# Performance work log

Hardware: AMD Instinct MI355X
Metric: run time of the kernel (lower is better)

## Reference

```python
import jax, jax.numpy as jnp
import numpy as np

B, N, E = 8, 4096, 1024
H = 16
D = E // H
NMAX = 4096
N_FFT = NMAX // 2 + 1  # 2049
HIDDEN = max(32, D)    # 64
LN_EPS = 1e-5


def setup_inputs() -> dict:
    key = jax.random.key(0)
    ks = jax.random.split(key, 8)
    s = 0.02
    return {
        "x": jax.random.normal(ks[0], (B, N, E), jnp.float32),
        "positions": jnp.arange(N, dtype=jnp.int64),
        "Wq": jax.random.normal(ks[1], (E, E), jnp.float32) * s,
        "Wv": jax.random.normal(ks[2], (E, E), jnp.float32) * s,
        "Wo": jax.random.normal(ks[3], (E, E), jnp.float32) * s,
        "ln_g": jnp.ones((D,), jnp.float32),
        "ln_b": jnp.zeros((D,), jnp.float32),
        "w1": jax.random.normal(ks[4], (HIDDEN, D), jnp.float32) * s,
        "b1": jnp.zeros((HIDDEN,), jnp.float32),
        "w2": jax.random.normal(ks[5], (2 * N_FFT, HIDDEN), jnp.float32) * s,
        "b2": jnp.zeros((2 * N_FFT,), jnp.float32),
    }


def _build_gate(bar_q, ln_g, ln_b, w1, b1, w2, b2):
    # bar_q: (B,H,D) -> complex gate (B,H,n_fft)
    mu = bar_q.mean(-1, keepdims=True)
    var = ((bar_q - mu) ** 2).mean(-1, keepdims=True)  # biased var (torch LayerNorm)
    h = (bar_q - mu) * jax.lax.rsqrt(var + LN_EPS) * ln_g + ln_b
    h = jax.nn.silu(h @ w1.T + b1)                      # (B,H,HIDDEN)
    g = (h @ w2.T + b2).reshape(bar_q.shape[0], H, N_FFT, 2)
    return jax.lax.complex(g[..., 0], g[..., 1])        # (B,H,n_fft)


def reference(x, positions, Wq, Wv, Wo, ln_g, ln_b, w1, b1, w2, b2):
    b, n, e = x.shape
    q = (x @ Wq.T).reshape(b, n, H, D).transpose(0, 2, 1, 3)  # (B,H,N,D)
    v = (x @ Wv.T).reshape(b, n, H, D).transpose(0, 2, 1, 3)  # (B,H,N,D)
    v_fft = jnp.fft.rfft(v, axis=2)                            # (B,H,n_fft,D) complex
    bar_q = q.mean(axis=2)                                     # (B,H,D)
    gate = _build_gate(bar_q, ln_g, ln_b, w1, b1, w2, b2)      # (B,H,n_fft)
    spec = v_fft * gate[..., None]
    seq_full = jnp.fft.irfft(spec, n=NMAX, axis=2)             # (B,H,Nmax,D)
    v_sel = jnp.take(seq_full, positions, axis=2)              # (B,H,N,D)
    v_out = v_sel.transpose(0, 2, 1, 3).reshape(b, n, e)
    return v_out @ Wo.T
```

## Files before the change

kernel.cpp:

```cpp
#include <hip/hip_runtime.h>
#include <cstdint>

#define B_   8
#define N_   4096
#define E_   1024
#define H_   16
#define NFFT 2049

typedef unsigned short u16;
typedef unsigned int   u32;
typedef __attribute__((ext_vector_type(4))) float f32x4;
typedef __attribute__((ext_vector_type(8))) short short8;

__device__ __forceinline__ u16 f2bf(float f) {
    u32 u = __builtin_bit_cast(u32, f);
    u += 0x7fffu + ((u >> 16) & 1u);
    return (u16)(u >> 16);
}
__device__ __forceinline__ float bf2f(u16 h) {
    u32 u = ((u32)h) << 16;
    return __builtin_bit_cast(float, u);
}

__global__ __launch_bounds__(256)
void conv_x_kernel(const float* __restrict__ x, u16* __restrict__ xbf,
                   float* __restrict__ xbar)
{
    const int b  = blockIdx.y;
    const int n0 = blockIdx.x * 64;
    const int t  = threadIdx.x;
    const float4* src = (const float4*)(x + ((size_t)(b * N_ + n0)) * E_) + t;
    u16* dst = xbf + ((size_t)(b * N_ + n0)) * E_ + t * 4;
    float4 s = make_float4(0.f, 0.f, 0.f, 0.f);
    for (int r = 0; r < 64; r++) {
        float4 v = src[r * 256];
        s.x += v.x; s.y += v.y; s.z += v.z; s.w += v.w;
        *(ushort4*)(dst + (size_t)r * E_) =
            make_ushort4(f2bf(v.x), f2bf(v.y), f2bf(v.z), f2bf(v.w));
    }
    float* xb = xbar + b * E_ + t * 4;
    atomicAdd(xb + 0, s.x); atomicAdd(xb + 1, s.y);
    atomicAdd(xb + 2, s.z); atomicAdd(xb + 3, s.w);
}

__global__ __launch_bounds__(256)
void convw_kernel(const float* __restrict__ w, u16* __restrict__ wbf, int n4)
{
    int i = blockIdx.x * 256 + threadIdx.x;
    if (i >= n4) return;
    float4 v = ((const float4*)w)[i];
    *(ushort4*)(wbf + (size_t)i * 4) =
        make_ushort4(f2bf(v.x), f2bf(v.y), f2bf(v.z), f2bf(v.w));
}

__global__ __launch_bounds__(256)
void gate_kernel(const float* __restrict__ xbar, const float* __restrict__ Wq,
                 const float* __restrict__ ln_g, const float* __restrict__ ln_b,
                 const float* __restrict__ w1,   const float* __restrict__ b1,
                 const float* __restrict__ w2,   const float* __restrict__ b2,
                 float* __restrict__ gate)
{
    const int bh = blockIdx.x;
    const int b = bh >> 4, h = bh & 15;
    const int t = threadIdx.x;
    __shared__ float s_x[1024];
    __shared__ float s_bq[64], s_ln[64], s_h1[64];

    for (int q = 0; q < 4; q++)
        s_x[(q << 8) + t] = xbar[b * 1024 + (q << 8) + t] * (1.0f / 4096.0f);
    __syncthreads();

    {
        const int d = t >> 2, part = t & 3;
        const float* wrow = Wq + (size_t)(h * 64 + d) * 1024 + part * 256;
        const float* xr = s_x + part * 256;
        float sum = 0.f;
        #pragma unroll 8
        for (int e = 0; e < 256; e++) sum += wrow[e] * xr[e];
        sum += __shfl_xor(sum, 1);
        sum += __shfl_xor(sum, 2);
        if (part == 0) s_bq[d] = sum;
    }
    __syncthreads();

    if (t < 64) {
        float v = s_bq[t];
        float s = v;
        #pragma unroll
        for (int m = 1; m < 64; m <<= 1) s += __shfl_xor(s, m);
        float mu = s * (1.0f / 64.0f);
        float dv = v - mu;
        float vv = dv * dv;
        #pragma unroll
        for (int m = 1; m < 64; m <<= 1) vv += __shfl_xor(vv, m);
        float var = vv * (1.0f / 64.0f);
        s_ln[t] = dv * rsqrtf(var + 1e-5f) * ln_g[t] + ln_b[t];
    }
    __syncthreads();

    {
        const int j = t >> 2, part = t & 3;
        const float* wrow = w1 + j * 64 + part * 16;
        const float* lr = s_ln + part * 16;
        float sum = 0.f;
        #pragma unroll
        for (int d2 = 0; d2 < 16; d2++) sum += wrow[d2] * lr[d2];
        sum += __shfl_xor(sum, 1);
        sum += __shfl_xor(sum, 2);
        if (part == 0) {
            float z = sum + b1[j];
            s_h1[j] = z / (1.0f + __expf(-z));
        }
    }
    __syncthreads();

    float* grow = gate + (size_t)bh * (2 * NFFT);
    for (int o = t; o < 2 * NFFT; o += 256) {
        const float4* wrow = (const float4*)(w2 + (size_t)o * 64);
        float sum = 0.f;
        #pragma unroll
        for (int d4 = 0; d4 < 16; d4++) {
            float4 wv = wrow[d4];
            sum += wv.x * s_h1[d4 * 4]     + wv.y * s_h1[d4 * 4 + 1]
                 + wv.z * s_h1[d4 * 4 + 2] + wv.w * s_h1[d4 * 4 + 3];
        }
        float gv = (sum + b2[o]) * (1.0f / 4096.0f);
        if (o == 1 || o == 2 * NFFT - 1) gv = 0.0f;
        grow[o] = gv;
    }
}

template<int OUTMODE>
__global__ __launch_bounds__(256)
void gemm_bt(const u16* __restrict__ A, const u16* __restrict__ BT,
             void* __restrict__ Cv, int M, int N, int K)
{
    __shared__ __align__(16) u16 lA[128 * 32];
    __shared__ __align__(16) u16 lB[128 * 32];
    const int tid = threadIdx.x;
    const int w = tid >> 6, l = tid & 63;
    const int m0 = blockIdx.y * 128, n0 = blockIdx.x * 128;
    const int wr = (w >> 1) * 64, wc = (w & 1) * 64;
    const int srow = w * 16 + (l >> 2);
    const int scol = (l & 3) * 8;
    const u16* ga = A  + (size_t)(m0 + srow) * K + scol;
    const u16* gb = BT + (size_t)(n0 + srow) * K + scol;
    char* lac = (char*)lA;
    char* lbc = (char*)lB;
    f32x4 acc[4][4] = {};

    short8 ra0 = *(const short8*)(ga);
    short8 ra1 = *(const short8*)(ga + (size_t)64 * K);
    short8 rb0 = *(const short8*)(gb);
    short8 rb1 = *(const short8*)(gb + (size_t)64 * K);

    for (int k0 = 0; k0 < K; k0 += 32) {
        __syncthreads();
        *(short8*)(lac +        w * 1024 + l * 16) = ra0;
        *(short8*)(lac + 4096 + w * 1024 + l * 16) = ra1;
        *(short8*)(lbc +        w * 1024 + l * 16) = rb0;
        *(short8*)(lbc + 4096 + w * 1024 + l * 16) = rb1;
        if (k0 + 32 < K) {
            ra0 = *(const short8*)(ga + k0 + 32);
            ra1 = *(const short8*)(ga + (size_t)64 * K + k0 + 32);
            rb0 = *(const short8*)(gb + k0 + 32);
            rb1 = *(const short8*)(gb + (size_t)64 * K + k0 + 32);
        }
        __syncthreads();
        short8 af[4], bfr[4];
        #pragma unroll
        for (int i = 0; i < 4; i++) {
            af[i]  = *(const short8*)(lac + (wr + i * 16 + (l & 15)) * 64 + (l >> 4) * 16);
            bfr[i] = *(const short8*)(lbc + (wc + i * 16 + (l & 15)) * 64 + (l >> 4) * 16);
        }
        #pragma unroll
        for (int i = 0; i < 4; i++)
            #pragma unroll
            for (int j2 = 0; j2 < 4; j2++)
                asm("v_mfma_f32_16x16x32_bf16 %0, %1, %2, %0"
                    : "+v"(acc[i][j2]) : "v"(af[i]), "v"(bfr[j2]));
    }

    const int fr = (l >> 4) * 4;
    const int fc = l & 15;
    if (OUTMODE == 0) {
        float* C = (float*)Cv;
        #pragma unroll
        for (int i = 0; i < 4; i++) {
            int m = m0 + wr + i * 16 + fr;
            #pragma unroll
            for (int j2 = 0; j2 < 4; j2++) {
                int gn = n0 + wc + j2 * 16 + fc;
                #pragma unroll
                for (int r = 0; r < 4; r++)
                    C[(size_t)(m + r) * N + gn] = acc[i][j2][r];
            }
        }
    } else {
        u16* Cb = (u16*)Cv;
        #pragma unroll
        for (int i = 0; i < 4; i++) {
            int m = m0 + wr + i * 16 + fr;
            #pragma unroll
            for (int j2 = 0; j2 < 4; j2++) {
                int gn = n0 + wc + j2 * 16 + fc;
                int bb = gn >> 12, nin = gn & 4095;
                size_t base = ((size_t)bb << 22) + (size_t)nin;
                #pragma unroll
                for (int r = 0; r < 4; r++)
                    Cb[base + (size_t)(m + r) * 4096] = f2bf(acc[i][j2][r]);
            }
        }
    }
}

__device__ __forceinline__ float2 cmul(float2 a, float2 b) {
    return make_float2(a.x * b.x - a.y * b.y, a.x * b.y + a.y * b.x);
}
__device__ __forceinline__ float2 cadd(float2 a, float2 b) {
    return make_float2(a.x + b.x, a.y + b.y);
}
__device__ __forceinline__ float2 csub(float2 a, float2 b) {
    return make_float2(a.x - b.x, a.y - b.y);
}

template<int SIGN>
__device__ __forceinline__ void fft6(float2* A, float2* B, int t)
{
    float2* x = A;
    float2* y = B;
    for (int s = 0; s < 6; s++) {
        const int Ns = 1 << (2 * s);
        const float inv = 1.0f / (float)(Ns << 2);
        #pragma unroll
        for (int q = 0; q < 4; q++) {
            int jj = t + (q << 8);
            int jm = jj & (Ns - 1);
            float ang = (SIGN * 6.283185307179586f) * (float)jm * inv;
            float sn, cs;
            __sincosf(ang, &sn, &cs);
            float2 w1 = make_float2(cs, sn);
            float2 w2 = cmul(w1, w1);
            float2 w3 = cmul(w2, w1);
            float2 v0 = x[jj];
            float2 v1 = cmul(x[jj + 1024], w1);
            float2 v2 = cmul(x[jj + 2048], w2);
            float2 v3 = cmul(x[jj + 3072], w3);
            float2 t0 = cadd(v0, v2), t1 = csub(v0, v2);
            float2 t2 = cadd(v1, v3), t3 = csub(v1, v3);
            float2 V0 = cadd(t0, t2), V2 = csub(t0, t2);
            float2 jt3;
            if (SIGN < 0) { jt3.x =  t3.y; jt3.y = -t3.x; }
            else          { jt3.x = -t3.y; jt3.y =  t3.x; }
            float2 V1 = cadd(t1, jt3), V3 = csub(t1, jt3);
            int idx = ((jj - jm) << 2) + jm;
            y[idx]          = V0;
            y[idx + Ns]     = V1;
            y[idx + 2 * Ns] = V2;
            y[idx + 3 * Ns] = V3;
        }
        __syncthreads();
        float2* tmp = x; x = y; y = tmp;
    }
}

__global__ __launch_bounds__(256)
void fft_conv(const u16* __restrict__ vt, const float2* __restrict__ gate,
              u16* __restrict__ yt)
{
    __shared__ float2 bufA[4096];
    __shared__ float2 bufB[4096];
    const int blk = blockIdx.x;
    const int b = blk >> 9;
    const int rem = blk & 511;
    const size_t rowoff = ((size_t)b * 1024 + rem * 2) * 4096;
    const u16* r0 = vt + rowoff;
    const u16* r1 = r0 + 4096;
    const int t = threadIdx.x;

    for (int q = 0; q < 16; q++) {
        int n = (q << 8) + t;
        bufA[n] = make_float2(bf2f(r0[n]), bf2f(r1[n]));
    }
    __syncthreads();

    fft6<-1>(bufA, bufB, t);

    const float2* grow = gate + (size_t)((b << 4) | (rem >> 5)) * NFFT;
    for (int q = 0; q < 16; q++) {
        int k = (q << 8) + t;
        float2 g;
        if (k <= 2048) g = grow[k];
        else { float2 gg = grow[4096 - k]; g.x = gg.x; g.y = -gg.y; }
        float2 z = bufA[k];
        bufA[k] = make_float2(z.x * g.x - z.y * g.y, z.x * g.y + z.y * g.x);
    }
    __syncthreads();

    fft6<1>(bufA, bufB, t);

    u16* o0 = yt + rowoff;
    u16* o1 = o0 + 4096;
    for (int q = 0; q < 16; q++) {
        int n = (q << 8) + t;
        float2 zz = bufA[n];
        o0[n] = f2bf(zz.x);
        o1[n] = f2bf(zz.y);
    }
}

__global__ __launch_bounds__(256)
void transpose_bn(const u16* __restrict__ in, u16* __restrict__ out)
{
    __shared__ u32 tile[64 * 65];
    const int b  = blockIdx.z;
    const int j0 = blockIdx.y << 6;
    const int n0 = blockIdx.x << 6;
    const int t  = threadIdx.x;
    #pragma unroll
    for (int i2 = 0; i2 < 16; i2++) {
        int el = (i2 << 8) + t;
        int jr = el >> 6, nc = el & 63;
        tile[jr * 65 + nc] = in[((size_t)b * 1024 + j0 + jr) * 4096 + n0 + nc];
    }
    __syncthreads();
    #pragma unroll
    for (int i2 = 0; i2 < 16; i2++) {
        int el = (i2 << 8) + t;
        int nr = el >> 6, jc = el & 63;
        out[((size_t)b * 4096 + n0 + nr) * 1024 + j0 + jc] = (u16)tile[jc * 65 + nr];
    }
}

extern "C" void kernel_launch(void* const* d_in, const int* in_sizes, int n_in,
                              void* d_out, int out_size, void* d_ws, size_t ws_size,
                              hipStream_t stream)
{
    (void)in_sizes; (void)n_in; (void)out_size; (void)ws_size;
    const float* x    = (const float*)d_in[0];
    const float* Wq   = (const float*)d_in[2];
    const float* Wv   = (const float*)d_in[3];
    const float* Wo   = (const float*)d_in[4];
    const float* ln_g = (const float*)d_in[5];
    const float* ln_b = (const float*)d_in[6];
    const float* w1   = (const float*)d_in[7];
    const float* b1   = (const float*)d_in[8];
    const float* w2   = (const float*)d_in[9];
    const float* b2   = (const float*)d_in[10];

    char* ws = (char*)d_ws;
    size_t off = 0;
    auto carve = [&](size_t bytes) -> char* {
        char* p = ws + off;
        off += (bytes + 255) & ~(size_t)255;
        return p;
    };
    u16*   x_bf  = (u16*)carve((size_t)B_ * N_ * E_ * 2);
    u16*   vt    = (u16*)carve((size_t)B_ * N_ * E_ * 2);
    u16*   Wv_bf = (u16*)carve((size_t)E_ * E_ * 2);
    u16*   Wo_bf = (u16*)carve((size_t)E_ * E_ * 2);
    float* xbar  = (float*)carve((size_t)B_ * E_ * 4);
    float* gate  = (float*)carve((size_t)B_ * H_ * NFFT * 8);
    u16* yt  = x_bf;
    u16* ybt = vt;

    hipMemsetAsync(xbar, 0, (size_t)B_ * E_ * 4, stream);
    conv_x_kernel<<<dim3(64, B_), 256, 0, stream>>>(x, x_bf, xbar);
    convw_kernel<<<dim3(1024), 256, 0, stream>>>(Wv, Wv_bf, 262144);
    convw_kernel<<<dim3(1024), 256, 0, stream>>>(Wo, Wo_bf, 262144);
    gate_kernel<<<dim3(128), 256, 0, stream>>>(xbar, Wq, ln_g, ln_b, w1, b1, w2, b2, gate);
    gemm_bt<1><<<dim3(256, 8), 256, 0, stream>>>(Wv_bf, x_bf, vt, 1024, 32768, 1024);
    fft_conv<<<dim3(4096), 256, 0, stream>>>(vt, (const float2*)gate, yt);
    transpose_bn<<<dim3(64, 16, B_), 256, 0, stream>>>(yt, ybt);
    gemm_bt<0><<<dim3(8, 256), 256, 0, stream>>>(ybt, Wo_bf, d_out, 32768, 1024, 1024);
}
```

Baseline: 635.0 us.

## Use register radix-16 FFT, direct-to-LDS GEMM loads and XCD block swizzle

New measurement: 560.4 us. 11.7% less time.

```diff
diff --git a/kernel.cpp b/kernel.cpp
--- a/kernel.cpp
+++ b/kernel.cpp
@@ -20,6 +20,13 @@
 __device__ __forceinline__ float bf2f(u16 h) {
     u32 u = ((u32)h) << 16;
     return __builtin_bit_cast(float, u);
+}
+
+__device__ __forceinline__ void gload16(const void* g, void* l) {
+    __builtin_amdgcn_global_load_lds(
+        (const __attribute__((address_space(1))) void*)(uintptr_t)g,
+        (__attribute__((address_space(3))) void*)(u32)(uintptr_t)l,
+        16, 0, 0);
 }
 
 __global__ __launch_bounds__(256)
@@ -133,45 +140,42 @@
 template<int OUTMODE>
 __global__ __launch_bounds__(256)
 void gemm_bt(const u16* __restrict__ A, const u16* __restrict__ BT,
-             void* __restrict__ Cv, int M, int N, int K)
+             void* __restrict__ Cv, int M, int N, int K,
+             int nbx_mask, int nbx_shift)
 {
     __shared__ __align__(16) u16 lA[128 * 32];
     __shared__ __align__(16) u16 lB[128 * 32];
     const int tid = threadIdx.x;
     const int w = tid >> 6, l = tid & 63;
-    const int m0 = blockIdx.y * 128, n0 = blockIdx.x * 128;
+    const int nwg = gridDim.x;
+    const int q = nwg >> 3;
+    const int bid = blockIdx.x;
+    const int swz = (bid & 7) * q + (bid >> 3);
+    const int bx = swz & nbx_mask, by = swz >> nbx_shift;
+    const int m0 = by * 128, n0 = bx * 128;
     const int wr = (w >> 1) * 64, wc = (w & 1) * 64;
     const int srow = w * 16 + (l >> 2);
     const int scol = (l & 3) * 8;
     const u16* ga = A  + (size_t)(m0 + srow) * K + scol;
     const u16* gb = BT + (size_t)(n0 + srow) * K + scol;
-    char* lac = (char*)lA;
-    char* lbc = (char*)lB;
+    u16* lAw0 = lA + w * 512;
+    u16* lAw1 = lA + 2048 + w * 512;
+    u16* lBw0 = lB + w * 512;
+    u16* lBw1 = lB + 2048 + w * 512;
     f32x4 acc[4][4] = {};
-
-    short8 ra0 = *(const short8*)(ga);
-    short8 ra1 = *(const short8*)(ga + (size_t)64 * K);
-    short8 rb0 = *(const short8*)(gb);
-    short8 rb1 = *(const short8*)(gb + (size_t)64 * K);
 
     for (int k0 = 0; k0 < K; k0 += 32) {
         __syncthreads();
-        *(short8*)(lac +        w * 1024 + l * 16) = ra0;
-        *(short8*)(lac + 4096 + w * 1024 + l * 16) = ra1;
-        *(short8*)(lbc +        w * 1024 + l * 16) = rb0;
-        *(short8*)(lbc + 4096 + w * 1024 + l * 16) = rb1;
-        if (k0 + 32 < K) {
-            ra0 = *(const short8*)(ga + k0 + 32);
-            ra1 = *(const short8*)(ga + (size_t)64 * K + k0 + 32);
-            rb0 = *(const short8*)(gb + k0 + 32);
-            rb1 = *(const short8*)(gb + (size_t)64 * K + k0 + 32);
-        }
+        gload16(ga + k0,                   lAw0);
+        gload16(ga + (size_t)64 * K + k0,  lAw1);
+        gload16(gb + k0,                   lBw0);
+        gload16(gb + (size_t)64 * K + k0,  lBw1);
         __syncthreads();
         short8 af[4], bfr[4];
         #pragma unroll
         for (int i = 0; i < 4; i++) {
-            af[i]  = *(const short8*)(lac + (wr + i * 16 + (l & 15)) * 64 + (l >> 4) * 16);
-            bfr[i] = *(const short8*)(lbc + (wc + i * 16 + (l & 15)) * 64 + (l >> 4) * 16);
+            af[i]  = *(const short8*)((char*)lA + (wr + i * 16 + (l & 15)) * 64 + (l >> 4) * 16);
+            bfr[i] = *(const short8*)((char*)lB + (wc + i * 16 + (l & 15)) * 64 + (l >> 4) * 16);
         }
         #pragma unroll
         for (int i = 0; i < 4; i++)
@@ -223,53 +227,69 @@
 __device__ __forceinline__ float2 csub(float2 a, float2 b) {
     return make_float2(a.x - b.x, a.y - b.y);
 }
-
-template<int SIGN>
-__device__ __forceinline__ void fft6(float2* A, float2* B, int t)
-{
-    float2* x = A;
-    float2* y = B;
-    for (int s = 0; s < 6; s++) {
-        const int Ns = 1 << (2 * s);
-        const float inv = 1.0f / (float)(Ns << 2);
-        #pragma unroll
-        for (int q = 0; q < 4; q++) {
-            int jj = t + (q << 8);
-            int jm = jj & (Ns - 1);
-            float ang = (SIGN * 6.283185307179586f) * (float)jm * inv;
-            float sn, cs;
-            __sincosf(ang, &sn, &cs);
-            float2 w1 = make_float2(cs, sn);
-            float2 w2 = cmul(w1, w1);
-            float2 w3 = cmul(w2, w1);
-            float2 v0 = x[jj];
-            float2 v1 = cmul(x[jj + 1024], w1);
-            float2 v2 = cmul(x[jj + 2048], w2);
-            float2 v3 = cmul(x[jj + 3072], w3);
-            float2 t0 = cadd(v0, v2), t1 = csub(v0, v2);
-            float2 t2 = cadd(v1, v3), t3 = csub(v1, v3);
-            float2 V0 = cadd(t0, t2), V2 = csub(t0, t2);
-            float2 jt3;
-            if (SIGN < 0) { jt3.x =  t3.y; jt3.y = -t3.x; }
-            else          { jt3.x = -t3.y; jt3.y =  t3.x; }
-            float2 V1 = cadd(t1, jt3), V3 = csub(t1, jt3);
-            int idx = ((jj - jm) << 2) + jm;
-            y[idx]          = V0;
-            y[idx + Ns]     = V1;
-            y[idx + 2 * Ns] = V2;
-            y[idx + 3 * Ns] = V3;
-        }
-        __syncthreads();
-        float2* tmp = x; x = y; y = tmp;
-    }
-}
-
-__global__ __launch_bounds__(256)
+__device__ __forceinline__ float2 cmulc(float2 z, float wr, float wi) {
+    return make_float2(z.x * wr - z.y * wi, z.x * wi + z.y * wr);
+}
+
+template<int SGN>
+__device__ __forceinline__ void dft16(float2* r)
+{
+    const float s = (float)SGN;
+    const float C1 = 0.9238795325112867f;
+    const float S1 = 0.3826834323650898f;
+    const float R2 = 0.7071067811865476f;
+    float2 Bv[16];
+    #pragma unroll
+    for (int j0 = 0; j0 < 4; j0++) {
+        float2 a = r[j0], b = r[4 + j0], c = r[8 + j0], d = r[12 + j0];
+        float2 t0 = cadd(a, c), t1 = csub(a, c);
+        float2 t2 = cadd(b, d), t3 = csub(b, d);
+        float2 rt = make_float2(-s * t3.y, s * t3.x);
+        Bv[j0 * 4 + 0] = cadd(t0, t2);
+        Bv[j0 * 4 + 1] = cadd(t1, rt);
+        Bv[j0 * 4 + 2] = csub(t0, t2);
+        Bv[j0 * 4 + 3] = csub(t1, rt);
+    }
+    Bv[5]  = cmulc(Bv[5],  C1,  s * S1);
+    Bv[6]  = cmulc(Bv[6],  R2,  s * R2);
+    Bv[7]  = cmulc(Bv[7],  S1,  s * C1);
+    Bv[9]  = cmulc(Bv[9],  R2,  s * R2);
+    Bv[10] = make_float2(-s * Bv[10].y, s * Bv[10].x);
+    Bv[11] = cmulc(Bv[11], -R2,  s * R2);
+    Bv[13] = cmulc(Bv[13],  S1,  s * C1);
+    Bv[14] = cmulc(Bv[14], -R2,  s * R2);
+    Bv[15] = cmulc(Bv[15], -C1, -s * S1);
+    #pragma unroll
+    for (int k0 = 0; k0 < 4; k0++) {
+        float2 a = Bv[k0], b = Bv[4 + k0], c = Bv[8 + k0], d = Bv[12 + k0];
+        float2 t0 = cadd(a, c), t1 = csub(a, c);
+        float2 t2 = cadd(b, d), t3 = csub(b, d);
+        float2 rt = make_float2(-s * t3.y, s * t3.x);
+        r[k0]      = cadd(t0, t2);
+        r[k0 + 4]  = cadd(t1, rt);
+        r[k0 + 8]  = csub(t0, t2);
+        r[k0 + 12] = csub(t1, rt);
+    }
+}
+
+__device__ __forceinline__ void twiddle_iter(float2* r, float ang)
+{
+    float sn, cs;
+    __sincosf(ang, &sn, &cs);
+    float2 w = make_float2(cs, sn);
+    float2 tw = w;
+    #pragma unroll
+    for (int m = 1; m < 16; m++) {
+        r[m] = cmul(r[m], tw);
+        tw = cmul(tw, w);
+    }
+}
+
+__global__ __launch_bounds__(256, 4)
 void fft_conv(const u16* __restrict__ vt, const float2* __restrict__ gate,
               u16* __restrict__ yt)
 {
-    __shared__ float2 bufA[4096];
-    __shared__ float2 bufB[4096];
+    __shared__ float2 S[4608];
     const int blk = blockIdx.x;
     const int b = blk >> 9;
     const int rem = blk & 511;
@@ -277,35 +297,85 @@
     const u16* r0 = vt + rowoff;
     const u16* r1 = r0 + 4096;
     const int t = threadIdx.x;
-
-    for (int q = 0; q < 16; q++) {
-        int n = (q << 8) + t;
-        bufA[n] = make_float2(bf2f(r0[n]), bf2f(r1[n]));
-    }
-    __syncthreads();
-
-    fft6<-1>(bufA, bufB, t);
-
+    const int k1 = t >> 4, j16 = t & 15;
+
+    float2 r[16];
+    #pragma unroll
+    for (int j = 0; j < 16; j++) {
+        int n = j * 256 + t;
+        r[j] = make_float2(bf2f(r0[n]), bf2f(r1[n]));
+    }
+    dft16<-1>(r);
+    twiddle_iter(r, -6.283185307179586f * (float)t * (1.0f / 4096.0f));
+    #pragma unroll
+    for (int m = 0; m < 16; m++)
+        S[m * 288 + t + 2 * (t >> 4)] = r[m];
+    __syncthreads();
+
+    {
+        int base = k1 * 288 + j16;
+        #pragma unroll
+        for (int j = 0; j < 16; j++) r[j] = S[base + 18 * j];
+        dft16<-1>(r);
+        twiddle_iter(r, -6.283185307179586f * (float)j16 * (1.0f / 256.0f));
+        #pragma unroll
+        for (int m = 0; m < 16; m++) S[base + 18 * m] = r[m];
+    }
+
+    const int d = k1 + (j16 << 4);
     const float2* grow = gate + (size_t)((b << 4) | (rem >> 5)) * NFFT;
-    for (int q = 0; q < 16; q++) {
-        int k = (q << 8) + t;
-        float2 g;
-        if (k <= 2048) g = grow[k];
-        else { float2 gg = grow[4096 - k]; g.x = gg.x; g.y = -gg.y; }
-        float2 z = bufA[k];
-        bufA[k] = make_float2(z.x * g.x - z.y * g.y, z.x * g.y + z.y * g.x);
-    }
-    __syncthreads();
-
-    fft6<1>(bufA, bufB, t);
+    float2 g[16];
+    #pragma unroll
+    for (int j = 0; j < 16; j++) {
+        int k = d + (j << 8);
+        bool hi = k > 2048;
+        int idx = hi ? 4096 - k : k;
+        float2 gg = grow[idx];
+        g[j] = make_float2(gg.x, hi ? -gg.y : gg.y);
+    }
+    __syncthreads();
+
+    {
+        int base = k1 * 288 + j16 * 18;
+        #pragma unroll
+        for (int j = 0; j < 16; j += 2) {
+            float4 v = *(const float4*)&S[base + j];
+            r[j]     = make_float2(v.x, v.y);
+            r[j + 1] = make_float2(v.z, v.w);
+        }
+        dft16<-1>(r);
+        #pragma unroll
+        for (int j = 0; j < 16; j++) r[j] = cmul(r[j], g[j]);
+        dft16<1>(r);
+        twiddle_iter(r, 6.283185307179586f * (float)j16 * (1.0f / 256.0f));
+        #pragma unroll
+        for (int m = 0; m < 16; m += 2)
+            *(float4*)&S[base + m] = make_float4(r[m].x, r[m].y, r[m + 1].x, r[m + 1].y);
+    }
+    __syncthreads();
+
+    {
+        int base = k1 * 288 + j16;
+        #pragma unroll
+        for (int j = 0; j < 16; j++) r[j] = S[base + 18 * j];
+        dft16<1>(r);
+        #pragma unroll
+        for (int m = 0; m < 16; m++) S[base + 18 * m] = r[m];
+    }
+    __syncthreads();
+
+    #pragma unroll
+    for (int j = 0; j < 16; j++) r[j] = S[j * 288 + t + 2 * (t >> 4)];
+    twiddle_iter(r, 6.283185307179586f * (float)t * (1.0f / 4096.0f));
+    dft16<1>(r);
 
     u16* o0 = yt + rowoff;
     u16* o1 = o0 + 4096;
-    for (int q = 0; q < 16; q++) {
-        int n = (q << 8) + t;
-        float2 zz = bufA[n];
-        o0[n] = f2bf(zz.x);
-        o1[n] = f2bf(zz.y);
+    #pragma unroll
+    for (int m = 0; m < 16; m++) {
+        int n = m * 256 + t;
+        o0[n] = f2bf(r[m].x);
+        o1[n] = f2bf(r[m].y);
     }
 }
 
@@ -369,8 +439,8 @@
     convw_kernel<<<dim3(1024), 256, 0, stream>>>(Wv, Wv_bf, 262144);
     convw_kernel<<<dim3(1024), 256, 0, stream>>>(Wo, Wo_bf, 262144);
     gate_kernel<<<dim3(128), 256, 0, stream>>>(xbar, Wq, ln_g, ln_b, w1, b1, w2, b2, gate);
-    gemm_bt<1><<<dim3(256, 8), 256, 0, stream>>>(Wv_bf, x_bf, vt, 1024, 32768, 1024);
+    gemm_bt<1><<<dim3(2048), 256, 0, stream>>>(Wv_bf, x_bf, vt, 1024, 32768, 1024, 255, 8);
     fft_conv<<<dim3(4096), 256, 0, stream>>>(vt, (const float2*)gate, yt);
     transpose_bn<<<dim3(64, 16, B_), 256, 0, stream>>>(yt, ybt);
-    gemm_bt<0><<<dim3(8, 256), 256, 0, stream>>>(ybt, Wo_bf, d_out, 32768, 1024, 1024);
-}
+    gemm_bt<0><<<dim3(2048), 256, 0, stream>>>(ybt, Wo_bf, d_out, 32768, 1024, 1024, 7, 3);
+}
```
